# Kernel optimization log

Measured on AMD Instinct MI355X. Metric: run time of the kernel, lower is better.

Reference implementation:

```python
import jax, jax.numpy as jnp
import numpy as np

EPS = 1e-5


def _conv1x1_3d(x, w, b):
    # x: [B,C,T,H,W], w: [O,C], b: [O]  (Conv3d with kernel 1)
    return jnp.einsum('bcthw,oc->bothw', x, w) + b[None, :, None, None, None]


def _nonlocal_layer(x, Kw, Kb, Qw, Qb, Vw, Vb, Ow, Ob, gamma, beta, in_dim):
    K = _conv1x1_3d(x, Kw, Kb)
    Q = _conv1x1_3d(x, Qw, Qb)
    V = _conv1x1_3d(x, Vw, Vb)
    B, C, T, H, W = K.shape
    S = T * H * W
    Kf = K.reshape(B, C, S)
    Qf = Q.reshape(B, C, S)
    Vf = V.reshape(B, C, S)
    # KQ[b,s,t] = sum_c K[b,c,s] Q[b,c,t];  attn = softmax over t
    attn = jax.nn.softmax(jnp.einsum('bcs,bct->bst', Kf, Qf) / np.sqrt(in_dim).astype(np.float32), axis=2)
    # original broadcast pattern: (V.view(B,C,S,1) * attn[:,None]).sum(3)
    #   == V[b,c,s] * sum_t attn[b,s,t]  (rows of softmax sum to ~1)
    Vn = Vf * attn.sum(axis=2)[:, None, :]
    Vn = jax.nn.relu(Vn).reshape(B, C, T, H, W)
    O = jax.nn.relu(_conv1x1_3d(Vn, Ow, Ob))
    y = x + O
    # BatchNorm3d in training mode: per-channel batch statistics
    mu = y.mean(axis=(0, 2, 3, 4), keepdims=True)
    var = y.var(axis=(0, 2, 3, 4), keepdims=True)
    return gamma[None, :, None, None, None] * (y - mu) / jnp.sqrt(var + EPS) + beta[None, :, None, None, None]


def _conv_transpose_2x2_s2(x, w, b):
    # torch ConvTranspose2d(k=2, stride=2): weight [Cin, Cout, 2, 2]; output pixels don't overlap
    N, C, H, W = x.shape
    O = w.shape[1]
    y = jnp.einsum('nchw,codk->nohdwk', x, w).reshape(N, O, 2 * H, 2 * W)
    return y + b[None, :, None, None]


def _positional_encoding(S, D):
    position = jnp.arange(S, dtype=jnp.float32)[:, None]
    div_term = jnp.exp(jnp.arange(0, D, 2, dtype=jnp.float32) * (-np.log(10000.0) / D))
    pe = jnp.zeros((S, D), dtype=jnp.float32)
    pe = pe.at[:, 0::2].set(jnp.sin(position * div_term))
    pe = pe.at[:, 1::2].set(jnp.cos(position * div_term))
    return pe  # [S, D]


def setup_inputs() -> dict:
    key = jax.random.key(0)
    ks = jax.random.split(key, 24)
    B, Tc, Hc, Wc = 8, 6, 12, 12
    Tf, Hf, Wf = 4, 12, 12
    Din, Dff, Dout, L = 1024, 512, 128, 2
    s = 0.02
    inp = {
        'context': jax.random.normal(ks[0], (B, Tc, Din, Hc, Wc), jnp.float32),
        'frame': jax.random.normal(ks[1], (B, Tf, Din, Hf, Wf), jnp.float32),
        'nl_Kw': jax.random.normal(ks[2], (L, Dff, Din), jnp.float32) * s,
        'nl_Kb': jnp.zeros((L, Dff), jnp.float32),
        'nl_Qw': jax.random.normal(ks[3], (L, Dff, Din), jnp.float32) * s,
        'nl_Qb': jnp.zeros((L, Dff), jnp.float32),
        'nl_Vw': jax.random.normal(ks[4], (L, Dff, Din), jnp.float32) * s,
        'nl_Vb': jnp.zeros((L, Dff), jnp.float32),
        'nl_Ow': jax.random.normal(ks[5], (L, Din, Dff), jnp.float32) * s,
        'nl_Ob': jnp.zeros((L, Din), jnp.float32),
        'nl_gamma': jnp.ones((L, Din), jnp.float32),
        'nl_beta': jnp.zeros((L, Din), jnp.float32),
        'tp_w': jax.random.normal(ks[6], (Dout, Din, 3, 3, 3), jnp.float32) * s,
        'tp_b': jnp.zeros((Dout,), jnp.float32),
        'up1_w': jax.random.normal(ks[7], (Din, Dff, 2, 2), jnp.float32) * s,
        'up1_b': jnp.zeros((Dff,), jnp.float32),
        'up2_w': jax.random.normal(ks[8], (Dff, Dout, 2, 2), jnp.float32) * s,
        'up2_b': jnp.zeros((Dout,), jnp.float32),
    }
    return inp


def reference(context, frame, nl_Kw, nl_Kb, nl_Qw, nl_Qb, nl_Vw, nl_Vb, nl_Ow, nl_Ob,
              nl_gamma, nl_beta, tp_w, tp_b, up1_w, up1_b, up2_w, up2_b):
    in_dim = context.shape[2]
    out_dim = up2_w.shape[1]
    # ---- non-local layers over context ----
    x = jnp.swapaxes(context, 1, 2)  # [B, C, T, H, W]
    n_layers = nl_Kw.shape[0]
    for l in range(n_layers):
        x = _nonlocal_layer(x, nl_Kw[l], nl_Kb[l], nl_Qw[l], nl_Qb[l], nl_Vw[l], nl_Vb[l],
                            nl_Ow[l], nl_Ob[l], nl_gamma[l], nl_beta[l], in_dim)
    # ---- temporal pool (Conv3d k=3, VALID) + ReLU + global avg pool ----
    g = jax.lax.conv_general_dilated(x, tp_w, (1, 1, 1), 'VALID',
                                     dimension_numbers=('NCDHW', 'OIDHW', 'NCDHW'))
    g = jax.nn.relu(g + tp_b[None, :, None, None, None])
    goal_embed = g.mean(axis=(2, 3, 4))  # [B, out_dim]
    # ---- upsample frame ----
    B, Tf, C, H, W = frame.shape
    fr = frame.reshape(B * Tf, C, H, W)
    h = jax.nn.relu(_conv_transpose_2x2_s2(fr, up1_w, up1_b))
    h = _conv_transpose_2x2_s2(h, up2_w, up2_b)  # [B*Tf, out_dim, 4H, 4W]
    N = B * Tf
    S = H * W * 16
    state_embed = h.reshape(N, out_dim, S)
    # ---- positional encoding on V ----
    pe = _positional_encoding(S, out_dim)  # [S, D]
    V = jnp.transpose(state_embed, (0, 2, 1)) + pe[None, :, :]  # [N, S, D]
    # ---- goal/state attention (note: torch .repeat tiles t-major, kept faithful) ----
    goal_rep = jnp.tile(goal_embed, (Tf, 1))  # [Tf*B, D], index t*B+b
    SG = jnp.einsum('nds,nd->ns', state_embed, goal_rep) / np.sqrt(out_dim).astype(np.float32)
    attn = jax.nn.softmax(SG, axis=1)  # [N, S]
    state_goal_attn = jnp.einsum('ns,nsd->nd', attn, V).reshape(B, Tf, out_dim)
    return (goal_embed, state_goal_attn)
```

## Files before the change

### kernel.cpp

```cpp
#include <hip/hip_runtime.h>
#include <cstddef>
#include <cstdint>


static constexpr int B_ = 8, TC = 6, TF = 4, DIN = 1024, DFF = 512, DOUT = 128;
static constexpr int HWP = 144;
static constexpr int P_CTX = B_ * TC * HWP;
static constexpr int NF = B_ * TF;
static constexpr int P_FRM = NF * HWP;
static constexpr int P_H1 = NF * 24 * 24;
static constexpr int P_H2 = NF * 48 * 48;
static constexpr int S2 = 48 * 48;
static constexpr int NPOS = 3200;

static constexpr size_t OFF_XB   = 0;
static constexpr size_t OFF_YB   = 3538944;
static constexpr size_t OFF_VNB  = 7077888;
static constexpr size_t OFF_WB1  = 8847360;
static constexpr size_t OFF_WB2  = 9371648;
static constexpr size_t OFF_ST   = 9895936;
static constexpr size_t OFF_TWB  = 9900032;
static constexpr size_t OFF_W1B  = 11669504;
static constexpr size_t OFF_W2B  = 12718080;
static constexpr size_t OFF_GP   = 12849152;
static constexpr size_t OFF_R    = 18378752;
static constexpr size_t OFF_HP1B = 18788352;
static constexpr size_t OFF_F0B  = 3538944;
static constexpr size_t OFF_HP2B = 0;
static constexpr size_t OFF_SG   = 12849152;
static constexpr size_t OFF_PP   = 12922880;
static constexpr size_t OFF_PE   = 13070336;

typedef __attribute__((ext_vector_type(8))) short bf16x8;
typedef __attribute__((ext_vector_type(4))) float f32x4;
typedef __attribute__((ext_vector_type(4))) unsigned short us4;
typedef __attribute__((ext_vector_type(8))) unsigned short us8;

__device__ __forceinline__ unsigned short f2b(float f) {
    union { float f; uint32_t u; } x{f};
    uint32_t r = x.u + 0x7FFFu + ((x.u >> 16) & 1u);
    return (unsigned short)(r >> 16);
}
__device__ __forceinline__ float b2f(unsigned short u) {
    union { uint32_t u; float f; } x;
    x.u = (uint32_t)u << 16;
    return x.f;
}

#define GL16(g, s)                                                        \
    __builtin_amdgcn_global_load_lds(                                     \
        (const __attribute__((address_space(1))) void*)(g),               \
        (__attribute__((address_space(3))) void*)(s), 16, 0, 0)


__global__ __launch_bounds__(256) void transpose_cm_pm(const float* __restrict__ in,
                                                       unsigned short* __restrict__ outB,
                                                       int C, int HW) {
    __shared__ float T[64][17];
    int tx = threadIdx.x, ty = threadIdx.y;
    int f = blockIdx.z, hw0 = blockIdx.x * 16, c0 = blockIdx.y * 64;
#pragma unroll
    for (int i = 0; i < 4; ++i)
        T[ty + 16 * i][tx] = in[((size_t)f * C + c0 + ty + 16 * i) * HW + hw0 + tx];
    __syncthreads();
#pragma unroll
    for (int i = 0; i < 4; ++i)
        outB[((size_t)f * HW + hw0 + ty) * C + c0 + tx + 16 * i] = f2b(T[tx + 16 * i][ty]);
}

static constexpr int PW0 = 4 * 524288;
static constexpr int PW1 = PW0 + 27 * 1024 * 128;
static constexpr int PW2 = PW1 + 4 * 512 * 1024;
static constexpr int PW3 = PW2 + 4 * 128 * 512;
__global__ __launch_bounds__(256) void prep_weights(
    const float* __restrict__ Vw, const float* __restrict__ Ow,
    const float* __restrict__ tp, const float* __restrict__ u1w,
    const float* __restrict__ u2w,
    unsigned short* __restrict__ WB1, unsigned short* __restrict__ WB2,
    unsigned short* __restrict__ TWB, unsigned short* __restrict__ W1B,
    unsigned short* __restrict__ W2B) {
    int t = blockIdx.x * 256 + threadIdx.x;
    if (t < PW0) {
        int which = t >> 19;
        int r = t & 524287;
        int kr = r & 7;
        int layer = which >> 1;
        if ((which & 1) == 0) {
            int o = (r >> 3) & 511, kg = (r >> 3) >> 9;
            WB1[(size_t)layer * 524288 + r] =
                f2b(Vw[(size_t)layer * 524288 + (size_t)o * 1024 + kg * 8 + kr]);
        } else {
            int o = (r >> 3) & 1023, kg = (r >> 3) >> 10;
            WB2[(size_t)layer * 524288 + r] =
                f2b(Ow[(size_t)layer * 524288 + (size_t)o * 512 + kg * 8 + kr]);
        }
    } else if (t < PW1) {
        int r = t - PW0;
        int kr = r & 7, o = (r >> 3) & 127, kg = (r >> 10) & 127, tap = r >> 17;
        int c = kg * 8 + kr;
        TWB[r] = f2b(tp[((size_t)o * 1024 + c) * 27 + tap]);
    } else if (t < PW2) {
        int r = t - PW1;
        int kr = r & 7, o = (r >> 3) % 512;
        int rest = (r >> 3) / 512;
        int kg = rest & 127, d = rest >> 7;
        W1B[r] = f2b(u1w[((size_t)(kg * 8 + kr) * 512 + o) * 4 + d]);
    } else if (t < PW3) {
        int r = t - PW2;
        int kr = r & 7, o = (r >> 3) & 127;
        int rest = (r >> 3) >> 7;
        int kg = rest & 63, d = rest >> 6;
        W2B[r] = f2b(u2w[((size_t)(kg * 8 + kr) * 128 + o) * 4 + d]);
    }
}

__global__ __launch_bounds__(256) void pe_table(float* __restrict__ PE) {
    int idx = blockIdx.x * 256 + threadIdx.x;
    int s = idx >> 7, d = idx & 127;
    float freq = expf(-(float)(d & ~1) * (9.210340371976184f / 128.f));
    float ang = (float)s * freq;
    PE[idx] = (d & 1) ? cosf(ang) : sinf(ang);
}

template <int EPI, int REMAP, int GATHER, int MT>
__device__ __forceinline__ void gemm_body(
    const unsigned short* __restrict__ A, const unsigned short* __restrict__ Bp,
    const float* __restrict__ bias, const unsigned short* __restrict__ resid,
    void* __restrict__ Cv, int M, int N, int K,
    size_t bStrideZ, size_t cStrideZ,
    int inW, int inHW, int outW, int outSPP,
    int bx, int by, int bz,
    unsigned short* AlP, unsigned short* BlP, int* sPix) {
    constexpr int MI = MT / 32;
    constexpr int AL = MT / 64;
    constexpr int ASZ = MT * 32;
    int tid = threadIdx.x;
    int w = tid >> 6, l = tid & 63;
    int m0 = by * MT, n0 = bx * 128;
    int z = bz;
    const unsigned short* Bpz = Bp + (size_t)z * bStrideZ;

    if (GATHER) {
        if (tid < MT) {
            int pos = m0 + tid;
            int ww = pos % 10;
            int r = pos / 10;
            int h = r % 10;
            r /= 10;
            int t = r & 3, b = r >> 2;
            int dt = z / 9, rr = z - dt * 9;
            int doff = dt * 144 + (rr / 3) * 12 + (rr % 3);
            sPix[tid] = ((b * 6 + t) * 12 + h) * 12 + ww + doff;
        }
        __syncthreads();
    }

    int wr = w >> 1, wc = w & 1;
    int l15 = l & 15, lg = l >> 4;

    float bv[4];
#pragma unroll
    for (int ni = 0; ni < 4; ++ni)
        bv[ni] = (EPI & 1) ? bias[n0 + wc * 64 + ni * 16 + l15] : 0.f;
    asm volatile("s_waitcnt vmcnt(0)" ::: "memory");

    const unsigned short* ag[AL];
    int aoff[AL];
#pragma unroll
    for (int a = 0; a < AL; ++a) {
        int row = l + a * 64;
        int grow = GATHER ? sPix[row] : (m0 + row);
        ag[a] = A + (size_t)grow * K + w * 8;
        aoff[a] = (w * MT + row) * 8;
    }
    int bkg = tid >> 7, bn = tid & 127;
    const unsigned short* bg0 = Bpz + ((size_t)bkg * N + n0 + bn) * 8;
    const unsigned short* bg1 = Bpz + ((size_t)(bkg + 2) * N + n0 + bn) * 8;
    const int boff0 = tid * 8, boff1 = (tid + 256) * 8;
    size_t bstep = (size_t)32 * N;

    f32x4 acc[MI][4];
#pragma unroll
    for (int mi = 0; mi < MI; ++mi)
#pragma unroll
        for (int ni = 0; ni < 4; ++ni) acc[mi][ni] = (f32x4){0.f, 0.f, 0.f, 0.f};

    int nt = K >> 5;
#pragma unroll
    for (int a = 0; a < AL; ++a) { GL16(ag[a], &AlP[aoff[a]]); ag[a] += 32; }
    GL16(bg0, &BlP[boff0]);
    GL16(bg1, &BlP[boff1]);
    bg0 += bstep; bg1 += bstep;
#pragma unroll
    for (int a = 0; a < AL; ++a) { GL16(ag[a], &AlP[ASZ + aoff[a]]); ag[a] += 32; }
    GL16(bg0, &BlP[4096 + boff0]);
    GL16(bg1, &BlP[4096 + boff1]);
    bg0 += bstep; bg1 += bstep;

    int bc = 0, sb = 2;
    for (int t = 0; t < nt; ++t) {
        __builtin_amdgcn_s_barrier();
        if (t + 2 < nt) {
#pragma unroll
            for (int a = 0; a < AL; ++a) { GL16(ag[a], &AlP[sb * ASZ + aoff[a]]); ag[a] += 32; }
            GL16(bg0, &BlP[sb * 4096 + boff0]);
            GL16(bg1, &BlP[sb * 4096 + boff1]);
            bg0 += bstep; bg1 += bstep;
            if (MT == 128)
                asm volatile("s_waitcnt vmcnt(8)" ::: "memory");
            else
                asm volatile("s_waitcnt vmcnt(6)" ::: "memory");
        } else if (t + 2 == nt) {
            if (MT == 128)
                asm volatile("s_waitcnt vmcnt(4)" ::: "memory");
            else
                asm volatile("s_waitcnt vmcnt(3)" ::: "memory");
        } else {
            asm volatile("s_waitcnt vmcnt(0)" ::: "memory");
        }
        __builtin_amdgcn_sched_barrier(0);
        bf16x8 af[MI], bf[4];
#pragma unroll
        for (int mi = 0; mi < MI; ++mi)
            af[mi] = *(const bf16x8*)&AlP[bc * ASZ + (lg * MT + wr * (MT / 2) + mi * 16 + l15) * 8];
#pragma unroll
        for (int ni = 0; ni < 4; ++ni)
            bf[ni] = *(const bf16x8*)&BlP[bc * 4096 + (lg * 128 + wc * 64 + ni * 16 + l15) * 8];
        __builtin_amdgcn_s_setprio(1);
#pragma unroll
        for (int mi = 0; mi < MI; ++mi)
#pragma unroll
            for (int ni = 0; ni < 4; ++ni)
                acc[mi][ni] = __builtin_amdgcn_mfma_f32_16x16x32_bf16(
                    af[mi], bf[ni], acc[mi][ni], 0, 0, 0);
        __builtin_amdgcn_s_setprio(0);
        __builtin_amdgcn_sched_barrier(0);
        bc = (bc == 2) ? 0 : bc + 1;
        sb = (sb == 2) ? 0 : sb + 1;
    }

    float* Cf = (float*)Cv + (size_t)z * cStrideZ;
    unsigned short* Cb = (unsigned short*)Cv + (size_t)z * cStrideZ;
#pragma unroll
    for (int mi = 0; mi < MI; ++mi) {
#pragma unroll
        for (int r = 0; r < 4; ++r) {
            int m = m0 + wr * (MT / 2) + mi * 16 + lg * 4 + r;
            int orow = m;
            if (REMAP) {
                int ni_ = m / inHW;
                int rem = m - ni_ * inHW;
                int h = rem / inW, ww = rem - h * inW;
                orow = ni_ * outSPP + (2 * h + (z >> 1)) * outW + (2 * ww + (z & 1));
            }
#pragma unroll
            for (int ni = 0; ni < 4; ++ni) {
                int n = n0 + wc * 64 + ni * 16 + l15;
                float v = acc[mi][ni][r] + bv[ni];
                if (EPI & 2) v = fmaxf(v, 0.f);
                if (EPI & 4) v += b2f(resid[(size_t)m * N + n]);
                if (EPI & 8)
                    Cb[(size_t)orow * N + n] = f2b(v);
                else
                    Cf[(size_t)orow * N + n] = v;
            }
        }
    }
}

template <int EPI, int REMAP, int GATHER, int MT>
__global__ __launch_bounds__(256) void gemm_mfma(
    const unsigned short* __restrict__ A, const unsigned short* __restrict__ Bp,
    const float* __restrict__ bias, const unsigned short* __restrict__ resid,
    void* __restrict__ Cv, int M, int N, int K,
    size_t bStrideZ, size_t cStrideZ,
    int inW, int inHW, int outW, int outSPP) {
    __shared__ unsigned short Al[3 * MT * 32];
    __shared__ unsigned short Bl[3 * 128 * 32];
    __shared__ int sPix[MT];
    gemm_body<EPI, REMAP, GATHER, MT>(A, Bp, bias, resid, Cv, M, N, K,
                                      bStrideZ, cStrideZ, inW, inHW, outW, outSPP,
                                      blockIdx.x, blockIdx.y, blockIdx.z,
                                      Al, Bl, sPix);
}

__global__ __launch_bounds__(256) void conv3_up1(
    const unsigned short* __restrict__ XB, const unsigned short* __restrict__ TWB,
    unsigned short* __restrict__ GP,
    const unsigned short* __restrict__ F0B, const unsigned short* __restrict__ W1B,
    const float* __restrict__ u1b, unsigned short* __restrict__ HP1B) {
    __shared__ unsigned short Al[3 * 128 * 32];
    __shared__ unsigned short Bl[3 * 128 * 32];
    __shared__ int sPix[128];
    if (blockIdx.x < 680) {
        int xcd = blockIdx.x & 7, k = blockIdx.x >> 3;
        int wcnt = (xcd < 3) ? 85 : 84;
        if (k >= wcnt) return;
        int wk = (xcd < 3) ? xcd * 85 + k : 255 + (xcd - 3) * 84 + k;
        gemm_body<8, 0, 1, 128>(XB, TWB, nullptr, nullptr, GP, NPOS, DOUT, DIN,
                                (size_t)DIN / 8 * DOUT * 8, (size_t)NPOS * DOUT,
                                0, 0, 0, 0, 0, wk / 27, wk % 27, Al, Bl, sPix);
    } else {
        int b = blockIdx.x - 680;
        gemm_body<11, 1, 0, 128>(F0B, W1B, u1b, nullptr, HP1B, P_FRM, DFF, DIN,
                                 (size_t)DIN / 8 * DFF * 8, 0, 12, 144, 24, 576,
                                 b & 3, (b >> 2) % 36, b / 144, Al, Bl, sPix);
    }
}


__global__ __launch_bounds__(256) void conv3_reduce(const unsigned short* __restrict__ Gp,
                                                    const float* __restrict__ bias,
                                                    float* __restrict__ R) {
    int idx = blockIdx.x * 256 + threadIdx.x;
    float s = 0.f;
    for (int tap = 0; tap < 27; ++tap) s += b2f(Gp[(size_t)tap * (NPOS * 128) + idx]);
    R[idx] = fmaxf(s + bias[idx & 127], 0.f);
}

__global__ __launch_bounds__(128) void goal_reduce(const float* __restrict__ R,
                                                   float* __restrict__ out) {
    int b = blockIdx.x, o = threadIdx.x;
    float s = 0.f;
    for (int i = 0; i < 400; ++i) s += R[(size_t)(b * 400 + i) * 128 + o];
    out[b * 128 + o] = s * (1.f / 400.f);
}


__global__ __launch_bounds__(256) void bn_stats_b(const unsigned short* __restrict__ YB,
                                                  float* __restrict__ st) {
    int tid = threadIdx.x;
    int p0 = blockIdx.x * 64;
    int c0 = tid * 4;
    float s[4] = {0, 0, 0, 0}, q[4] = {0, 0, 0, 0};
    for (int pp = 0; pp < 64; ++pp) {
        us4 y = *(const us4*)(YB + (size_t)(p0 + pp) * 1024 + c0);
#pragma unroll
        for (int j = 0; j < 4; ++j) {
            float v = b2f(y[j]);
            s[j] += v;
            q[j] += v * v;
        }
    }
#pragma unroll
    for (int j = 0; j < 4; ++j) {
        atomicAdd(&st[c0 + j], s[j]);
        atomicAdd(&st[1024 + c0 + j], q[j]);
    }
}

__global__ __launch_bounds__(256) void bn_final(float* __restrict__ st,
                                                const float* __restrict__ gamma,
                                                const float* __restrict__ beta) {
    int c = blockIdx.x * 256 + threadIdx.x;
    if (c >= 1024) return;
    const float invn = 1.f / 6912.f;
    float mean = st[c] * invn;
    float var = st[1024 + c] * invn - mean * mean;
    float sc = gamma[c] * rsqrtf(var + 1e-5f);
    st[2048 + c] = sc;
    st[3072 + c] = beta[c] - mean * sc;
}

__global__ __launch_bounds__(256) void bn_apply_b(const unsigned short* __restrict__ YB,
                                                  unsigned short* __restrict__ XB,
                                                  const float* __restrict__ st) {
    const float* scale = st + 2048;
    const float* shift = st + 3072;
    int idx = blockIdx.x * 256 + threadIdx.x;
    int c0 = (idx & 255) << 2;
    us4 y = ((const us4*)YB)[idx];
    us4 o;
#pragma unroll
    for (int j = 0; j < 4; ++j) o[j] = f2b(b2f(y[j]) * scale[c0 + j] + shift[c0 + j]);
    ((us4*)XB)[idx] = o;
}


__global__ __launch_bounds__(256) void attn_logits(const unsigned short* __restrict__ Hp2,
                                                   const float* __restrict__ out,
                                                   float* __restrict__ SG) {
    int n = blockIdx.y;
    int tid = threadIdx.x;
    int s = blockIdx.x * 16 + (tid >> 4);
    int l16 = tid & 15;
    us8 row = *((const us8*)(Hp2 + ((size_t)n * S2 + s) * 128) + l16);
    const float* g = out + (n & 7) * 128 + l16 * 8;
    float dot = 0.f;
#pragma unroll
    for (int i = 0; i < 8; ++i) dot += b2f(row[i]) * g[i];
    dot += __shfl_xor(dot, 1);
    dot += __shfl_xor(dot, 2);
    dot += __shfl_xor(dot, 4);
    dot += __shfl_xor(dot, 8);
    if (l16 == 0) SG[(size_t)n * S2 + s] = dot * 0.0883883476483184f;
}

__global__ __launch_bounds__(256) void attn_softmax(float* __restrict__ SG) {
    __shared__ float red[256];
    int n = blockIdx.x, tid = threadIdx.x;
    float* row = SG + (size_t)n * S2;
    float v[9];
    float lmax = -3.4e38f;
#pragma unroll
    for (int i = 0; i < 9; ++i) {
        v[i] = row[tid + 256 * i];
        lmax = fmaxf(lmax, v[i]);
    }
    red[tid] = lmax;
    __syncthreads();
    for (int off = 128; off > 0; off >>= 1) {
        if (tid < off) red[tid] = fmaxf(red[tid], red[tid + off]);
        __syncthreads();
    }
    float m = red[0];
    __syncthreads();
    float ls = 0.f;
#pragma unroll
    for (int i = 0; i < 9; ++i) {
        v[i] = expf(v[i] - m);
        ls += v[i];
    }
    red[tid] = ls;
    __syncthreads();
    for (int off = 128; off > 0; off >>= 1) {
        if (tid < off) red[tid] += red[tid + off];
        __syncthreads();
    }
    float inv = 1.f / red[0];
#pragma unroll
    for (int i = 0; i < 9; ++i) row[tid + 256 * i] = v[i] * inv;
}

__global__ __launch_bounds__(256) void attn_pv(const unsigned short* __restrict__ Hp2,
                                               const float* __restrict__ SG,
                                               const float* __restrict__ PE,
                                               float* __restrict__ PP) {
    int n = blockIdx.y;
    int sb = blockIdx.x;
    int tid = threadIdx.x;
    int d = tid & 127, half = tid >> 7;
    int s0 = sb * 128 + half * 64;
    const float* att = SG + (size_t)n * S2;
    float acc = 0.f;
    for (int i = 0; i < 64; ++i) {
        int s = s0 + i;
        acc += att[s] * (b2f(Hp2[((size_t)n * S2 + s) * 128 + d]) + PE[(size_t)s * 128 + d]);
    }
    PP[((size_t)n * 18 + sb) * 256 + tid] = acc;
}

__global__ __launch_bounds__(128) void attn_pv_reduce(const float* __restrict__ PP,
                                                      float* __restrict__ out) {
    int n = blockIdx.x, d = threadIdx.x;
    float s = 0.f;
    for (int i = 0; i < 18; ++i) {
        const float* p = PP + ((size_t)n * 18 + i) * 256;
        s += p[d] + p[128 + d];
    }
    out[1024 + n * 128 + d] = s;
}


extern "C" void kernel_launch(void* const* d_in, const int* in_sizes, int n_in,
                              void* d_out, int out_size, void* d_ws, size_t ws_size,
                              hipStream_t stream) {
    const float* context = (const float*)d_in[0];
    const float* frame = (const float*)d_in[1];
    const float* Vw = (const float*)d_in[6];
    const float* Vb = (const float*)d_in[7];
    const float* Ow = (const float*)d_in[8];
    const float* Ob = (const float*)d_in[9];
    const float* gamma = (const float*)d_in[10];
    const float* beta = (const float*)d_in[11];
    const float* tpw = (const float*)d_in[12];
    const float* tpb = (const float*)d_in[13];
    const float* u1w = (const float*)d_in[14];
    const float* u1b = (const float*)d_in[15];
    const float* u2w = (const float*)d_in[16];
    const float* u2b = (const float*)d_in[17];
    float* ws = (float*)d_ws;
    float* out = (float*)d_out;

    unsigned short* XB = (unsigned short*)(ws + OFF_XB);
    unsigned short* YB = (unsigned short*)(ws + OFF_YB);
    unsigned short* VNB = (unsigned short*)(ws + OFF_VNB);
    unsigned short* WB1 = (unsigned short*)(ws + OFF_WB1);
    unsigned short* WB2 = (unsigned short*)(ws + OFF_WB2);
    float* ST = ws + OFF_ST;
    unsigned short* TWB = (unsigned short*)(ws + OFF_TWB);
    unsigned short* W1B = (unsigned short*)(ws + OFF_W1B);
    unsigned short* W2B = (unsigned short*)(ws + OFF_W2B);
    unsigned short* GP = (unsigned short*)(ws + OFF_GP);
    float* R = ws + OFF_R;
    unsigned short* F0B = (unsigned short*)(ws + OFF_F0B);
    unsigned short* HP1B = (unsigned short*)(ws + OFF_HP1B);
    unsigned short* HP2B = (unsigned short*)(ws + OFF_HP2B);
    float* SG = ws + OFF_SG;
    float* PP = ws + OFF_PP;
    float* PE = ws + OFF_PE;

    prep_weights<<<PW3 / 256, 256, 0, stream>>>(Vw, Ow, tpw, u1w, u2w,
                                                WB1, WB2, TWB, W1B, W2B);
    transpose_cm_pm<<<dim3(HWP / 16, DIN / 64, B_ * TC), dim3(16, 16), 0, stream>>>(
        context, XB, DIN, HWP);

    for (int l = 0; l < 2; ++l) {
        gemm_mfma<11, 0, 0, 64><<<dim3(DFF / 128, P_CTX / 64, 1), 256, 0, stream>>>(
            XB, WB1 + (size_t)l * 524288, Vb + l * DFF, nullptr, VNB,
            P_CTX, DFF, DIN, 0, 0, 0, 0, 0, 0);
        gemm_mfma<15, 0, 0, 128><<<dim3(DIN / 128, P_CTX / 128, 1), 256, 0, stream>>>(
            VNB, WB2 + (size_t)l * 524288, Ob + l * DIN, XB, YB,
            P_CTX, DIN, DFF, 0, 0, 0, 0, 0, 0);
        hipMemsetAsync(ST, 0, 2048 * sizeof(float), stream);
        bn_stats_b<<<P_CTX / 64, 256, 0, stream>>>(YB, ST);
        bn_final<<<4, 256, 0, stream>>>(ST, gamma + l * DIN, beta + l * DIN);
        bn_apply_b<<<(P_CTX * DIN / 4) / 256, 256, 0, stream>>>(YB, XB, ST);
    }

    transpose_cm_pm<<<dim3(HWP / 16, DIN / 64, NF), dim3(16, 16), 0, stream>>>(
        frame, F0B, DIN, HWP);

    conv3_up1<<<680 + 576, 256, 0, stream>>>(XB, TWB, GP, F0B, W1B, u1b, HP1B);
    conv3_reduce<<<(NPOS * DOUT) / 256, 256, 0, stream>>>(GP, tpb, R);
    goal_reduce<<<8, 128, 0, stream>>>(R, out);
    pe_table<<<(S2 * 128) / 256, 256, 0, stream>>>(PE);

    gemm_mfma<9, 1, 0, 128><<<dim3(DOUT / 128, P_H1 / 128, 4), 256, 0, stream>>>(
        HP1B, W2B, u2b, nullptr, HP2B, P_H1, DOUT, DFF,
        (size_t)DFF / 8 * DOUT * 8, 0, 24, 576, 48, 2304);

    attn_logits<<<dim3(S2 / 16, NF), 256, 0, stream>>>(HP2B, out, SG);
    attn_softmax<<<NF, 256, 0, stream>>>(SG);
    attn_pv<<<dim3(18, NF), 256, 0, stream>>>(HP2B, SG, PE, PP);
    attn_pv_reduce<<<NF, 128, 0, stream>>>(PP, out);
}
```

Baseline: 302.3 us.

## Merge prep, transpose, reduce and PE kernels into fewer launches; atomic PV reduce

Combines weight prep with both input transposes into one launch, and merges the second upsample GEMM, the conv3 tap reduction and the PE table into one launch. The attention PV partial-sum buffer and its reduce kernel are replaced by atomicAdd into the zeroed output. This cuts kernel launch count and dependency serialization, and lets independent work share the GPU. The cost is workspace offset reshuffling, a memset, and float atomics that make the summation order nondeterministic.

Measured after the change: 286.4 us. 5.3% less time.

```diff
diff --git a/kernel.cpp b/kernel.cpp
--- a/kernel.cpp
+++ b/kernel.cpp
@@ -25,11 +25,10 @@
 static constexpr size_t OFF_GP   = 12849152;
 static constexpr size_t OFF_R    = 18378752;
 static constexpr size_t OFF_HP1B = 18788352;
-static constexpr size_t OFF_F0B  = 3538944;
+static constexpr size_t OFF_F0B  = 23506944;
 static constexpr size_t OFF_HP2B = 0;
 static constexpr size_t OFF_SG   = 12849152;
-static constexpr size_t OFF_PP   = 12922880;
-static constexpr size_t OFF_PE   = 13070336;
+static constexpr size_t OFF_PE   = 7077888;
 
 typedef __attribute__((ext_vector_type(8))) short bf16x8;
 typedef __attribute__((ext_vector_type(4))) float f32x4;
@@ -52,74 +51,82 @@
         (const __attribute__((address_space(1))) void*)(g),               \
         (__attribute__((address_space(3))) void*)(s), 16, 0, 0)
 
-
-__global__ __launch_bounds__(256) void transpose_cm_pm(const float* __restrict__ in,
-                                                       unsigned short* __restrict__ outB,
-                                                       int C, int HW) {
-    __shared__ float T[64][17];
-    int tx = threadIdx.x, ty = threadIdx.y;
-    int f = blockIdx.z, hw0 = blockIdx.x * 16, c0 = blockIdx.y * 64;
-#pragma unroll
-    for (int i = 0; i < 4; ++i)
-        T[ty + 16 * i][tx] = in[((size_t)f * C + c0 + ty + 16 * i) * HW + hw0 + tx];
-    __syncthreads();
-#pragma unroll
-    for (int i = 0; i < 4; ++i)
-        outB[((size_t)f * HW + hw0 + ty) * C + c0 + tx + 16 * i] = f2b(T[tx + 16 * i][ty]);
-}
-
 static constexpr int PW0 = 4 * 524288;
 static constexpr int PW1 = PW0 + 27 * 1024 * 128;
 static constexpr int PW2 = PW1 + 4 * 512 * 1024;
 static constexpr int PW3 = PW2 + 4 * 128 * 512;
-__global__ __launch_bounds__(256) void prep_weights(
+static constexpr int NB_PREP = PW3 / 256;
+static constexpr int NB_CTXT = 9 * 16 * (B_ * TC);
+static constexpr int NB_FRMT = 9 * 16 * NF;
+
+__device__ __forceinline__ void transpose_body(const float* __restrict__ in,
+                                               unsigned short* __restrict__ outB,
+                                               int C, int HW, int bx, int by, int bz,
+                                               float (*T)[17]) {
+    int tid = threadIdx.x;
+    int tx = tid & 15, ty = tid >> 4;
+    int f = bz, hw0 = bx * 16, c0 = by * 64;
+#pragma unroll
+    for (int i = 0; i < 4; ++i)
+        T[ty + 16 * i][tx] = in[((size_t)f * C + c0 + ty + 16 * i) * HW + hw0 + tx];
+    __syncthreads();
+#pragma unroll
+    for (int i = 0; i < 4; ++i)
+        outB[((size_t)f * HW + hw0 + ty) * C + c0 + tx + 16 * i] = f2b(T[tx + 16 * i][ty]);
+}
+
+__global__ __launch_bounds__(256) void prep_all(
     const float* __restrict__ Vw, const float* __restrict__ Ow,
     const float* __restrict__ tp, const float* __restrict__ u1w,
     const float* __restrict__ u2w,
+    const float* __restrict__ context, const float* __restrict__ frame,
     unsigned short* __restrict__ WB1, unsigned short* __restrict__ WB2,
     unsigned short* __restrict__ TWB, unsigned short* __restrict__ W1B,
-    unsigned short* __restrict__ W2B) {
-    int t = blockIdx.x * 256 + threadIdx.x;
-    if (t < PW0) {
-        int which = t >> 19;
-        int r = t & 524287;
-        int kr = r & 7;
-        int layer = which >> 1;
-        if ((which & 1) == 0) {
-            int o = (r >> 3) & 511, kg = (r >> 3) >> 9;
-            WB1[(size_t)layer * 524288 + r] =
-                f2b(Vw[(size_t)layer * 524288 + (size_t)o * 1024 + kg * 8 + kr]);
-        } else {
-            int o = (r >> 3) & 1023, kg = (r >> 3) >> 10;
-            WB2[(size_t)layer * 524288 + r] =
-                f2b(Ow[(size_t)layer * 524288 + (size_t)o * 512 + kg * 8 + kr]);
+    unsigned short* __restrict__ W2B,
+    unsigned short* __restrict__ XB, unsigned short* __restrict__ F0B) {
+    __shared__ float T[64][17];
+    int b = blockIdx.x;
+    if (b < NB_PREP) {
+        int t = b * 256 + threadIdx.x;
+        if (t < PW0) {
+            int which = t >> 19;
+            int r = t & 524287;
+            int kr = r & 7;
+            int layer = which >> 1;
+            if ((which & 1) == 0) {
+                int o = (r >> 3) & 511, kg = (r >> 3) >> 9;
+                WB1[(size_t)layer * 524288 + r] =
+                    f2b(Vw[(size_t)layer * 524288 + (size_t)o * 1024 + kg * 8 + kr]);
+            } else {
+                int o = (r >> 3) & 1023, kg = (r >> 3) >> 10;
+                WB2[(size_t)layer * 524288 + r] =
+                    f2b(Ow[(size_t)layer * 524288 + (size_t)o * 512 + kg * 8 + kr]);
+            }
+        } else if (t < PW1) {
+            int r = t - PW0;
+            int kr = r & 7, o = (r >> 3) & 127, kg = (r >> 10) & 127, tap = r >> 17;
+            int c = kg * 8 + kr;
+            TWB[r] = f2b(tp[((size_t)o * 1024 + c) * 27 + tap]);
+        } else if (t < PW2) {
+            int r = t - PW1;
+            int kr = r & 7, o = (r >> 3) % 512;
+            int rest = (r >> 3) / 512;
+            int kg = rest & 127, d = rest >> 7;
+            W1B[r] = f2b(u1w[((size_t)(kg * 8 + kr) * 512 + o) * 4 + d]);
+        } else if (t < PW3) {
+            int r = t - PW2;
+            int kr = r & 7, o = (r >> 3) & 127;
+            int rest = (r >> 3) >> 7;
+            int kg = rest & 63, d = rest >> 6;
+            W2B[r] = f2b(u2w[((size_t)(kg * 8 + kr) * 128 + o) * 4 + d]);
         }
-    } else if (t < PW1) {
-        int r = t - PW0;
-        int kr = r & 7, o = (r >> 3) & 127, kg = (r >> 10) & 127, tap = r >> 17;
-        int c = kg * 8 + kr;
-        TWB[r] = f2b(tp[((size_t)o * 1024 + c) * 27 + tap]);
-    } else if (t < PW2) {
-        int r = t - PW1;
-        int kr = r & 7, o = (r >> 3) % 512;
-        int rest = (r >> 3) / 512;
-        int kg = rest & 127, d = rest >> 7;
-        W1B[r] = f2b(u1w[((size_t)(kg * 8 + kr) * 512 + o) * 4 + d]);
-    } else if (t < PW3) {
-        int r = t - PW2;
-        int kr = r & 7, o = (r >> 3) & 127;
-        int rest = (r >> 3) >> 7;
-        int kg = rest & 63, d = rest >> 6;
-        W2B[r] = f2b(u2w[((size_t)(kg * 8 + kr) * 128 + o) * 4 + d]);
-    }
-}
-
-__global__ __launch_bounds__(256) void pe_table(float* __restrict__ PE) {
-    int idx = blockIdx.x * 256 + threadIdx.x;
-    int s = idx >> 7, d = idx & 127;
-    float freq = expf(-(float)(d & ~1) * (9.210340371976184f / 128.f));
-    float ang = (float)s * freq;
-    PE[idx] = (d & 1) ? cosf(ang) : sinf(ang);
+    } else if (b < NB_PREP + NB_CTXT) {
+        int bb = b - NB_PREP;
+        transpose_body(context, XB, DIN, HWP, bb % 9, (bb / 9) % 16, bb / 144, T);
+    } else {
+        int bb = b - NB_PREP - NB_CTXT;
+        transpose_body(frame, F0B, DIN, HWP, bb % 9, (bb / 9) % 16, bb / 144, T);
+    }
 }
 
 template <int EPI, int REMAP, int GATHER, int MT>
@@ -308,14 +315,31 @@
     }
 }
 
-
-__global__ __launch_bounds__(256) void conv3_reduce(const unsigned short* __restrict__ Gp,
-                                                    const float* __restrict__ bias,
-                                                    float* __restrict__ R) {
-    int idx = blockIdx.x * 256 + threadIdx.x;
-    float s = 0.f;
-    for (int tap = 0; tap < 27; ++tap) s += b2f(Gp[(size_t)tap * (NPOS * 128) + idx]);
-    R[idx] = fmaxf(s + bias[idx & 127], 0.f);
+__global__ __launch_bounds__(256) void up2_tail(
+    const unsigned short* __restrict__ HP1B, const unsigned short* __restrict__ W2B,
+    const float* __restrict__ u2b, unsigned short* __restrict__ HP2B,
+    const unsigned short* __restrict__ Gp, const float* __restrict__ tpb,
+    float* __restrict__ R, float* __restrict__ PE) {
+    __shared__ unsigned short Al[3 * 128 * 32];
+    __shared__ unsigned short Bl[3 * 128 * 32];
+    __shared__ int sPix[128];
+    int b = blockIdx.x;
+    if (b < 576) {
+        gemm_body<9, 1, 0, 128>(HP1B, W2B, u2b, nullptr, HP2B, P_H1, DOUT, DFF,
+                                (size_t)DFF / 8 * DOUT * 8, 0, 24, 576, 48, 2304,
+                                0, b % 144, b / 144, Al, Bl, sPix);
+    } else if (b < 2176) {
+        int idx = (b - 576) * 256 + threadIdx.x;
+        float s = 0.f;
+        for (int tap = 0; tap < 27; ++tap) s += b2f(Gp[(size_t)tap * (NPOS * 128) + idx]);
+        R[idx] = fmaxf(s + tpb[idx & 127], 0.f);
+    } else {
+        int idx = (b - 2176) * 256 + threadIdx.x;
+        int s = idx >> 7, d = idx & 127;
+        float freq = expf(-(float)(d & ~1) * (9.210340371976184f / 128.f));
+        float ang = (float)s * freq;
+        PE[idx] = (d & 1) ? cosf(ang) : sinf(ang);
+    }
 }
 
 __global__ __launch_bounds__(128) void goal_reduce(const float* __restrict__ R,
@@ -435,7 +459,7 @@
 __global__ __launch_bounds__(256) void attn_pv(const unsigned short* __restrict__ Hp2,
                                                const float* __restrict__ SG,
                                                const float* __restrict__ PE,
-                                               float* __restrict__ PP) {
+                                               float* __restrict__ out) {
     int n = blockIdx.y;
     int sb = blockIdx.x;
     int tid = threadIdx.x;
@@ -447,18 +471,7 @@
         int s = s0 + i;
         acc += att[s] * (b2f(Hp2[((size_t)n * S2 + s) * 128 + d]) + PE[(size_t)s * 128 + d]);
     }
-    PP[((size_t)n * 18 + sb) * 256 + tid] = acc;
-}
-
-__global__ __launch_bounds__(128) void attn_pv_reduce(const float* __restrict__ PP,
-                                                      float* __restrict__ out) {
-    int n = blockIdx.x, d = threadIdx.x;
-    float s = 0.f;
-    for (int i = 0; i < 18; ++i) {
-        const float* p = PP + ((size_t)n * 18 + i) * 256;
-        s += p[d] + p[128 + d];
-    }
-    out[1024 + n * 128 + d] = s;
+    atomicAdd(&out[1024 + n * 128 + d], acc);
 }
 
 
@@ -497,13 +510,10 @@
     unsigned short* HP1B = (unsigned short*)(ws + OFF_HP1B);
     unsigned short* HP2B = (unsigned short*)(ws + OFF_HP2B);
     float* SG = ws + OFF_SG;
-    float* PP = ws + OFF_PP;
     float* PE = ws + OFF_PE;
 
-    prep_weights<<<PW3 / 256, 256, 0, stream>>>(Vw, Ow, tpw, u1w, u2w,
-                                                WB1, WB2, TWB, W1B, W2B);
-    transpose_cm_pm<<<dim3(HWP / 16, DIN / 64, B_ * TC), dim3(16, 16), 0, stream>>>(
-        context, XB, DIN, HWP);
+    prep_all<<<NB_PREP + NB_CTXT + NB_FRMT, 256, 0, stream>>>(
+        Vw, Ow, tpw, u1w, u2w, context, frame, WB1, WB2, TWB, W1B, W2B, XB, F0B);
 
     for (int l = 0; l < 2; ++l) {
         gemm_mfma<11, 0, 0, 64><<<dim3(DFF / 128, P_CTX / 64, 1), 256, 0, stream>>>(
@@ -518,20 +528,14 @@
         bn_apply_b<<<(P_CTX * DIN / 4) / 256, 256, 0, stream>>>(YB, XB, ST);
     }
 
-    transpose_cm_pm<<<dim3(HWP / 16, DIN / 64, NF), dim3(16, 16), 0, stream>>>(
-        frame, F0B, DIN, HWP);
-
     conv3_up1<<<680 + 576, 256, 0, stream>>>(XB, TWB, GP, F0B, W1B, u1b, HP1B);
-    conv3_reduce<<<(NPOS * DOUT) / 256, 256, 0, stream>>>(GP, tpb, R);
+
+    up2_tail<<<576 + 1600 + 1152, 256, 0, stream>>>(HP1B, W2B, u2b, HP2B,
+                                                    GP, tpb, R, PE);
     goal_reduce<<<8, 128, 0, stream>>>(R, out);
-    pe_table<<<(S2 * 128) / 256, 256, 0, stream>>>(PE);
-
-    gemm_mfma<9, 1, 0, 128><<<dim3(DOUT / 128, P_H1 / 128, 4), 256, 0, stream>>>(
-        HP1B, W2B, u2b, nullptr, HP2B, P_H1, DOUT, DFF,
-        (size_t)DFF / 8 * DOUT * 8, 0, 24, 576, 48, 2304);
+    hipMemsetAsync(out + 1024, 0, (size_t)NF * 128 * sizeof(float), stream);
 
     attn_logits<<<dim3(S2 / 16, NF), 256, 0, stream>>>(HP2B, out, SG);
     attn_softmax<<<NF, 256, 0, stream>>>(SG);
-    attn_pv<<<dim3(18, NF), 256, 0, stream>>>(HP2B, SG, PE, PP);
-    attn_pv_reduce<<<NF, 128, 0, stream>>>(PP, out);
-}
+    attn_pv<<<dim3(18, NF), 256, 0, stream>>>(HP2B, SG, PE, out);
+}
```
